# Optimization experiments

Measured on AMD Instinct MI355X. Metric: run time of the kernel, lower is better.

## Reference

```python
import jax, jax.numpy as jnp
import numpy as np

# ---- geometry constants (from init_kwargs) ----
ANGLE_NUM = 360
DET = 448          # detector bins
N = 320            # volume is N x N, voxel pitch 1.0, centered at origin
SID = 500.0        # source-isocenter distance
SDD = 1000.0       # source-detector distance
DU = 1.6           # detector pixel pitch
LAMB = 1.0
R = N * np.sqrt(2.0) / 2.0   # half-diagonal of volume
N_SAMP = 452                 # samples per ray, step ~ 1 voxel
DT = np.float32(2.0 * R / N_SAMP)


def forward_project(vol):
    """Ray-driven fan-beam forward projection. vol: [B,N,N] -> sino [B,A,D]."""
    half = (N - 1) / 2.0
    betas = jnp.deg2rad(jnp.linspace(0.0, 360.0, ANGLE_NUM, endpoint=False)).astype(jnp.float32)
    u = ((jnp.arange(DET, dtype=jnp.float32) - (DET - 1) / 2.0) * DU)          # [D]
    t = (SID - R) + (jnp.arange(N_SAMP, dtype=jnp.float32) + 0.5) * (2.0 * R / N_SAMP)  # [S]

    def one_angle(_, beta):
        cb, sb = jnp.cos(beta), jnp.sin(beta)
        src = jnp.stack([SID * cb, SID * sb])            # source position [2]
        ax = jnp.stack([-cb, -sb])                       # toward isocenter
        uax = jnp.stack([-sb, cb])                       # detector axis
        det_pts = src[None, :] + SDD * ax[None, :] + u[:, None] * uax[None, :]  # [D,2]
        dirs = det_pts - src[None, :]
        dirs = dirs / jnp.linalg.norm(dirs, axis=-1, keepdims=True)             # [D,2]
        pts = src[None, None, :] + t[None, :, None] * dirs[:, None, :]          # [D,S,2]
        ix = pts[..., 0] + half
        iy = pts[..., 1] + half
        x0 = jnp.floor(ix); y0 = jnp.floor(iy)
        fx = ix - x0;       fy = iy - y0
        x0i = x0.astype(jnp.int32); y0i = y0.astype(jnp.int32)

        def gather(yy, xx):
            inb = (xx >= 0) & (xx < N) & (yy >= 0) & (yy < N)
            v = vol[:, jnp.clip(yy, 0, N - 1), jnp.clip(xx, 0, N - 1)]  # [B,D,S]
            return v * inb[None].astype(vol.dtype)

        val = (gather(y0i, x0i)         * ((1 - fx) * (1 - fy))[None]
             + gather(y0i, x0i + 1)     * (fx * (1 - fy))[None]
             + gather(y0i + 1, x0i)     * ((1 - fx) * fy)[None]
             + gather(y0i + 1, x0i + 1) * (fx * fy)[None])
        return None, val.sum(-1) * DT   # line integral per detector bin [B,D]

    _, sino = jax.lax.scan(one_angle, None, betas)   # [A,B,D]
    return jnp.transpose(sino, (1, 0, 2))            # [B,A,D]


def setup_inputs() -> dict:
    key = jax.random.key(0)
    k1, k2 = jax.random.split(key)
    x = jax.random.normal(k1, (2, N, N), dtype=jnp.float32)
    p = jax.random.normal(k2, (2, ANGLE_NUM, DET), dtype=jnp.float32)
    return {"x": x, "p": p}


def reference(x, p):
    # SART-style update: x - lamb * BP(FP(x) - p), BP = exact adjoint of FP
    residual = forward_project(x) - p
    (bp_vol,) = jax.linear_transpose(forward_project, x)(residual)
    return x - LAMB * bp_vol
```

## Files before the change

### kernel.cpp

```cpp
#include <hip/hip_runtime.h>
#include <hip/hip_fp16.h>
#include <math.h>

#define A_NUM 360
#define DET_N 448
#define NN 320
#define NSAMP 452
#define NB 2
#define NPIX (NN * NN)
#define NRAY (A_NUM * DET_N)
#define NCH 4
#define CHS (NSAMP / NCH)
#define NORB 25600
#define NSPQ15 15
#define NSPQ12 12
#define PN 324

#define R_D   226.27416997969522
#define DT_D  (2.0 * R_D / (double)NSAMP)
#define T0_D  (500.0 - R_D + 0.5 * DT_D)
#define DTF   ((float)DT_D)
#define T0F   ((float)T0_D)
#define INVDT ((float)(1.0 / DT_D))
#define K0F   ((float)((-1.4150 - T0_D) * (1.0 / DT_D)))

typedef float f32x2 __attribute__((ext_vector_type(2)));

__device__ __forceinline__ int orb_swizzle(int ri, int rj) {
    int tile = (rj >> 3) * 20 + (ri >> 3);
    int intra = ((rj & 7) << 3) | (ri & 7);
    return (tile << 6) | intra;
}

__global__ __launch_bounds__(256) void prep_k(float2* __restrict__ tabD,
                                              float4* __restrict__ tabS,
                                              float4* __restrict__ dirq,
                                              float4* __restrict__ angG) {
    int tid = blockIdx.x * blockDim.x + threadIdx.x;
    if (tid >= NRAY) return;
    int d = tid % DET_N, a = tid / DET_N;
    double beta = (double)a * (M_PI / 180.0);
    double cbd = cos(beta), sbd = sin(beta);
    double u = ((double)d - 223.5) * 1.6;
    double inorm = 1.0 / sqrt(1.0e6 + u * u);
    float dx = (float)((-1000.0 * cbd - u * sbd) * inorm);
    float dy = (float)((-1000.0 * sbd + u * cbd) * inorm);
    tabD[tid] = make_float2(dx, dy);
    if (d == 0) {
        tabS[a] = make_float4((float)cbd, (float)sbd,
                              (float)(500.0 * cbd + 161.5),
                              (float)(500.0 * sbd + 161.5));
        angG[a] = make_float4((float)cbd, (float)sbd,
                              (float)(500.0 * cbd + 159.5),
                              (float)(500.0 * sbd + 159.5));
    }
    if (a < 90) dirq[a * DET_N + d] = make_float4(dx, dy, DTF * dx, DTF * dy);
}

__device__ __forceinline__ unsigned packpix(const float* __restrict__ x,
                                            bool v, int idx) {
    if (!v) return 0u;
    __half2 h = __floats2half2_rn(x[idx], x[NPIX + idx]);
    return *reinterpret_cast<unsigned*>(&h);
}
__device__ __forceinline__ f32x2 up16(unsigned w) {
    __half2 h = *reinterpret_cast<__half2*>(&w);
    return (f32x2){__low2float(h), __high2float(h)};
}

__global__ __launch_bounds__(256) void interleaveQB_k(const float* __restrict__ x,
                                                      uint4* __restrict__ xb) {
    int t = blockIdx.x * blockDim.x + threadIdx.x;
    if (t >= PN * PN) return;
    int px = t % PN, py = t / PN;
    int ox = px - 2, oy = py - 2;
    bool cx0 = (ox >= 0) && (ox < NN);
    bool cx1 = (ox + 1 >= 0) && (ox + 1 < NN);
    bool cy0 = (oy >= 0) && (oy < NN);
    bool cy1 = (oy + 1 >= 0) && (oy + 1 < NN);
    int b = oy * NN + ox;
    uint4 w;
    w.x = packpix(x, cx0 && cy0, b);
    w.y = packpix(x, cx1 && cy0, b + 1);
    w.z = packpix(x, cx0 && cy1, b + NN);
    w.w = packpix(x, cx1 && cy1, b + NN + 1);
    xb[t] = w;
}

__global__ __launch_bounds__(256) void interleaveQBT_k(const float* __restrict__ x,
                                                       uint4* __restrict__ xbT) {
    int t = blockIdx.x * blockDim.x + threadIdx.x;
    if (t >= PN * PN) return;
    int r = t % PN, q = t / PN;
    int row0 = r - 2, col0 = q - 2;
    bool r0v = (row0 >= 0) && (row0 < NN);
    bool r1v = (row0 + 1 >= 0) && (row0 + 1 < NN);
    bool c0v = (col0 >= 0) && (col0 < NN);
    bool c1v = (col0 + 1 >= 0) && (col0 + 1 < NN);
    int b = row0 * NN + col0;
    uint4 w;
    w.x = packpix(x, r0v && c0v, b);
    w.y = packpix(x, r1v && c0v, b + NN);
    w.z = packpix(x, r0v && c1v, b + 1);
    w.w = packpix(x, r1v && c1v, b + NN + 1);
    xbT[t] = w;
}

__device__ __forceinline__ void samp1(const uint4* __restrict__ buf,
                                      float ix, float iy,
                                      f32x2& accA, f32x2& accB) {
    float xf = floorf(ix), yf = floorf(iy);
    float fx = ix - xf, fy = iy - yf;
    int idx = (int)yf * PN + (int)xf;
    uint4 qv = buf[idx];
    float gx = 1.0f - fx, gy = 1.0f - fy;
    float w00 = gx * gy, w01 = fx * gy, w10 = gx * fy, w11 = fx * fy;
    accA = __builtin_elementwise_fma((f32x2){w00, w00}, up16(qv.x), accA);
    accB = __builtin_elementwise_fma((f32x2){w01, w01}, up16(qv.y), accB);
    accA = __builtin_elementwise_fma((f32x2){w10, w10}, up16(qv.z), accA);
    accB = __builtin_elementwise_fma((f32x2){w11, w11}, up16(qv.w), accB);
}

__global__ __launch_bounds__(256) void partial_k(const float2* __restrict__ tabD,
                                                 const float4* __restrict__ tabS,
                                                 const uint4* __restrict__ bufR,
                                                 const uint4* __restrict__ bufT,
                                                 float2* __restrict__ part) {
    int tid = blockIdx.x * blockDim.x + threadIdx.x;
    if (tid >= NRAY * NCH) return;
    int d_lo = tid & 15;
    int c    = (tid >> 4) & 3;
    int rest = tid >> 6;
    int d_hi = rest % (DET_N / 16);
    int a    = rest / (DET_N / 16);
    int ray  = a * DET_N + d_hi * 16 + d_lo;

    float2 D = tabD[ray];
    float4 S = tabS[a];
    bool swp = fabsf(S.x) > fabsf(S.y);
    float dirx = swp ? D.y : D.x;
    float diry = swp ? D.x : D.y;
    float sx   = swp ? S.w : S.z;
    float sy   = swp ? S.z : S.w;
    const uint4* __restrict__ buf = swp ? bufT : bufR;

    float invx = __builtin_amdgcn_rcpf(dirx);
    float invy = __builtin_amdgcn_rcpf(diry);
    float tx1 = (0.5f   - sx) * invx;
    float tx2 = (322.5f - sx) * invx;
    float ty1 = (0.5f   - sy) * invy;
    float ty2 = (322.5f - sy) * invy;
    float tmn = fmaxf(fminf(tx1, tx2), fminf(ty1, ty2));
    float tmx = fminf(fmaxf(tx1, tx2), fmaxf(ty1, ty2));
    float smnf = fminf(fmaxf(ceilf((tmn - T0F) * INVDT), 0.0f), (float)(NSAMP - 1));
    float smxf = fminf(fmaxf(floorf((tmx - T0F) * INVDT), 0.0f), (float)(NSAMP - 1));
    int smin = (int)smnf;
    int smax = (int)smxf;
    int klo = (smin - c + 3) >> 2;  if (klo < 0) klo = 0;
    int khi = (smax - c) >> 2;      if (khi > CHS - 1) khi = CHS - 1;
    int kn = khi - klo + 1;

    float t0c = fmaf((float)(c + 4 * klo), DTF, T0F);
    float ix = fmaf(t0c, dirx, sx);
    float iy = fmaf(t0c, diry, sy);
    float stx = (4.0f * DTF) * dirx;
    float sty = (4.0f * DTF) * diry;

    f32x2 accA = {0.0f, 0.0f}, accB = {0.0f, 0.0f};

    int k = 0;
#pragma unroll 2
    for (; k + 4 <= kn; k += 4) {
        float ix0 = ix,              iy0 = iy;
        float ix1 = ix + stx,        iy1 = iy + sty;
        float ix2 = ix + 2.0f * stx, iy2 = iy + 2.0f * sty;
        float ix3 = ix + 3.0f * stx, iy3 = iy + 3.0f * sty;
        float xf0 = floorf(ix0), yf0 = floorf(iy0);
        float xf1 = floorf(ix1), yf1 = floorf(iy1);
        float xf2 = floorf(ix2), yf2 = floorf(iy2);
        float xf3 = floorf(ix3), yf3 = floorf(iy3);
        int i0 = (int)yf0 * PN + (int)xf0;
        int i1 = (int)yf1 * PN + (int)xf1;
        int i2 = (int)yf2 * PN + (int)xf2;
        int i3 = (int)yf3 * PN + (int)xf3;
        uint4 q0 = buf[i0];
        uint4 q1 = buf[i1];
        uint4 q2 = buf[i2];
        uint4 q3 = buf[i3];
        float fx0 = ix0 - xf0, fy0 = iy0 - yf0;
        float fx1 = ix1 - xf1, fy1 = iy1 - yf1;
        float fx2 = ix2 - xf2, fy2 = iy2 - yf2;
        float fx3 = ix3 - xf3, fy3 = iy3 - yf3;
        float gx0 = 1.0f - fx0, gy0 = 1.0f - fy0;
        float gx1 = 1.0f - fx1, gy1 = 1.0f - fy1;
        float gx2 = 1.0f - fx2, gy2 = 1.0f - fy2;
        float gx3 = 1.0f - fx3, gy3 = 1.0f - fy3;
        float w;
        w = gx0 * gy0; accA = __builtin_elementwise_fma((f32x2){w, w}, up16(q0.x), accA);
        w = fx0 * gy0; accB = __builtin_elementwise_fma((f32x2){w, w}, up16(q0.y), accB);
        w = gx0 * fy0; accA = __builtin_elementwise_fma((f32x2){w, w}, up16(q0.z), accA);
        w = fx0 * fy0; accB = __builtin_elementwise_fma((f32x2){w, w}, up16(q0.w), accB);
        w = gx1 * gy1; accA = __builtin_elementwise_fma((f32x2){w, w}, up16(q1.x), accA);
        w = fx1 * gy1; accB = __builtin_elementwise_fma((f32x2){w, w}, up16(q1.y), accB);
        w = gx1 * fy1; accA = __builtin_elementwise_fma((f32x2){w, w}, up16(q1.z), accA);
        w = fx1 * fy1; accB = __builtin_elementwise_fma((f32x2){w, w}, up16(q1.w), accB);
        w = gx2 * gy2; accA = __builtin_elementwise_fma((f32x2){w, w}, up16(q2.x), accA);
        w = fx2 * gy2; accB = __builtin_elementwise_fma((f32x2){w, w}, up16(q2.y), accB);
        w = gx2 * fy2; accA = __builtin_elementwise_fma((f32x2){w, w}, up16(q2.z), accA);
        w = fx2 * fy2; accB = __builtin_elementwise_fma((f32x2){w, w}, up16(q2.w), accB);
        w = gx3 * gy3; accA = __builtin_elementwise_fma((f32x2){w, w}, up16(q3.x), accA);
        w = fx3 * gy3; accB = __builtin_elementwise_fma((f32x2){w, w}, up16(q3.y), accB);
        w = gx3 * fy3; accA = __builtin_elementwise_fma((f32x2){w, w}, up16(q3.z), accA);
        w = fx3 * fy3; accB = __builtin_elementwise_fma((f32x2){w, w}, up16(q3.w), accB);
        ix += 4.0f * stx; iy += 4.0f * sty;
    }
    for (; k < kn; ++k) {
        samp1(buf, ix, iy, accA, accB);
        ix += stx; iy += sty;
    }

    f32x2 acc = accA + accB;
    part[c * NRAY + ray] = make_float2(acc.x, acc.y);
}

__global__ __launch_bounds__(256) void finalize4_k(const float* __restrict__ p,
                                                   const float2* __restrict__ part,
                                                   float4* __restrict__ rvq) {
    int tid = blockIdx.x * blockDim.x + threadIdx.x;
    if (tid >= 90 * DET_N) return;
    int d = tid % DET_N, am = tid / DET_N;
    float rv[8];
#pragma unroll
    for (int k = 0; k < 4; ++k) {
        int ray = (am + 90 * k) * DET_N + d;
        float a0 = 0.0f, a1 = 0.0f;
#pragma unroll
        for (int c = 0; c < NCH; ++c) {
            float2 pr = part[c * NRAY + ray];
            a0 += pr.x; a1 += pr.y;
        }
        rv[2 * k]     = -fmaf(a0, DTF, -p[ray]) * DTF;
        rv[2 * k + 1] = -fmaf(a1, DTF, -p[NRAY + ray]) * DTF;
    }
    rvq[2 * tid]     = make_float4(rv[0], rv[1], rv[2], rv[3]);
    rvq[2 * tid + 1] = make_float4(rv[4], rv[5], rv[6], rv[7]);
}

#define TAP4(A0, A1, A2, A3)                                 \
    {                                                        \
        f32x2 ad  = __builtin_elementwise_max(dxy, -dxy);    \
        f32x2 wv2 = __builtin_elementwise_max(one2 - ad, zero2); \
        float w = wv2.x * wv2.y;                             \
        f32x2 wv = {w, w};                                   \
        A0 = __builtin_elementwise_fma(wv, q0, A0);          \
        A1 = __builtin_elementwise_fma(wv, q1, A1);          \
        A2 = __builtin_elementwise_fma(wv, q2, A2);          \
        A3 = __builtin_elementwise_fma(wv, q3, A3);          \
        dxy += dd2;                                          \
    }

#define QBODY(A0, A1, A2, A3, Q, DX_, DY_, EX_, EY_)                       \
    for (int am = sp; am < 90; am += NSPLIT) {                             \
        int a = 90 * (Q) + am;                                             \
        float4 A = ang[a];                                                 \
        float rx = fi - A.z, ry = fj - A.w;                                \
        float rpar  = -fmaf(rx, A.x, ry * A.y);                            \
        float rperp = fmaf(ry, A.x, -rx * A.y);                            \
        float us = 1000.0f * rperp * __builtin_amdgcn_rcpf(rpar);          \
        float dstar = fmaf(us, 0.625f, 223.5f);                            \
        float r2 = fmaf(rx, rx, ry * ry);                                  \
        float ir = rsqrtf(r2);                                             \
        float g  = fmaf(fabsf(rx) + fabsf(ry), ir, 0.031f);                \
        float kk = fmaf(us, us, 1.0e6f) * ir;                              \
        float dd = fmaf(g * kk, 6.25e-4f, 0.05f);                          \
        int dlo = (int)ceilf(dstar - dd);  if (dlo < 0) dlo = 0;           \
        int dhi = (int)floorf(dstar + dd); if (dhi > DET_N - 1) dhi = DET_N - 1; \
        const float4* Drow = dirq + am * DET_N;                            \
        const float4* Rrow = rvq + am * DET_N * 2;                         \
        for (int d = dlo; d <= dhi; ++d) {                                 \
            float4 Dq  = Drow[d];                                          \
            float4 r01 = Rrow[2 * d];                                      \
            float4 r23 = Rrow[2 * d + 1];                                  \
            float Tx = DX_, Ty = DY_;                                      \
            float ts = fmaf(rx, Tx, ry * Ty);                              \
            float sf = ceilf(fmaf(ts, INVDT, K0F));                        \
            sf = fminf(fmaxf(sf, 0.0f), (float)(NSAMP - 3));               \
            float tt = fmaf(sf, DTF, T0F);                                 \
            f32x2 dxy = {fmaf(tt, Tx, -rx), fmaf(tt, Ty, -ry)};            \
            f32x2 dd2 = {EX_, EY_};                                        \
            f32x2 q0 = {r01.x, r01.y}, q1 = {r01.z, r01.w};                \
            f32x2 q2 = {r23.x, r23.y}, q3 = {r23.z, r23.w};                \
            TAP4(A0, A1, A2, A3)                                           \
            TAP4(A0, A1, A2, A3)                                           \
            TAP4(A0, A1, A2, A3)                                           \
        }                                                                  \
    }

template <int NSPLIT>
__global__ __launch_bounds__(256) void bp4_k(const float4* __restrict__ dirq,
                                             const float4* __restrict__ rvq,
                                             const float4* __restrict__ angG,
                                             float* __restrict__ bpp) {
    __shared__ float4 ang[A_NUM];
    for (int a = threadIdx.x; a < A_NUM; a += blockDim.x) ang[a] = angG[a];
    __syncthreads();

    int tid = blockIdx.x * blockDim.x + threadIdx.x;
    if (tid >= NORB * NSPLIT) return;
    int orb = tid % NORB;
    int sp  = tid / NORB;
    int tile  = orb >> 6;
    int intra = orb & 63;
    int ri = (tile % 20) * 8 + (intra & 7);
    int rj = (tile / 20) * 8 + (intra >> 3);
    float fi = (float)ri, fj = (float)rj;

    const f32x2 one2 = {1.0f, 1.0f}, zero2 = {0.0f, 0.0f};
    f32x2 acc0 = {0.0f, 0.0f}, acc1 = acc0, acc2 = acc0, acc3 = acc0;

    QBODY(acc0, acc1, acc2, acc3, 0,  Dq.x,  Dq.y,  Dq.z,  Dq.w)
    QBODY(acc3, acc0, acc1, acc2, 1, -Dq.y,  Dq.x, -Dq.w,  Dq.z)
    QBODY(acc2, acc3, acc0, acc1, 2, -Dq.x, -Dq.y, -Dq.z, -Dq.w)
    QBODY(acc1, acc2, acc3, acc0, 3,  Dq.y, -Dq.x,  Dq.w, -Dq.z)

    int base = sp * 8 * NORB + orb;
    bpp[base           ] = acc0.x;
    bpp[base + 1 * NORB] = acc0.y;
    bpp[base + 2 * NORB] = acc1.x;
    bpp[base + 3 * NORB] = acc1.y;
    bpp[base + 4 * NORB] = acc2.x;
    bpp[base + 5 * NORB] = acc2.y;
    bpp[base + 6 * NORB] = acc3.x;
    bpp[base + 7 * NORB] = acc3.y;
}

template <int NSPLIT>
__global__ __launch_bounds__(256) void combine4_k(const float* __restrict__ x,
                                                  const float* __restrict__ bpp,
                                                  float* __restrict__ out) {
    int tid = blockIdx.x * blockDim.x + threadIdx.x;
    if (tid >= NB * NPIX) return;
    int i = tid % NN;
    int j = (tid / NN) % NN;
    int b = tid / NPIX;
    int k, ri, rj;
    if (j < 160) {
        if (i < 160) { k = 0; ri = i;       rj = j;       }
        else         { k = 1; ri = j;       rj = 319 - i; }
    } else {
        if (i >= 160){ k = 2; ri = 319 - i; rj = 319 - j; }
        else         { k = 3; ri = 319 - j; rj = i;       }
    }
    int off = (k * 2 + b) * NORB + orb_swizzle(ri, rj);
    float s = x[tid];
#pragma unroll
    for (int sp = 0; sp < NSPLIT; ++sp) s += bpp[sp * 8 * NORB + off];
    out[tid] = s;
}

template <bool USE_TAB>
__global__ __launch_bounds__(256) void residual_k(const float* __restrict__ x,
                                                  const float* __restrict__ p,
                                                  void* __restrict__ tabv) {
    int tid = blockIdx.x * blockDim.x + threadIdx.x;
    if (tid >= NRAY) return;
    int d = tid % DET_N, a = tid / DET_N;
    double beta = (double)a * (M_PI / 180.0);
    double cbd = cos(beta), sbd = sin(beta);
    double u = ((double)d - 223.5) * 1.6;
    double inorm = 1.0 / sqrt(1.0e6 + u * u);
    float dirx = (float)((-1000.0 * cbd - u * sbd) * inorm);
    float diry = (float)((-1000.0 * sbd + u * cbd) * inorm);
    float sx = (float)(500.0 * cbd + 159.5);
    float sy = (float)(500.0 * sbd + 159.5);
    const float* __restrict__ v0 = x;
    const float* __restrict__ v1 = x + NPIX;
    float acc0 = 0.0f, acc1 = 0.0f;
    for (int s = 0; s < NSAMP; ++s) {
        float t  = fmaf((float)s, DTF, T0F);
        float ix = fmaf(t, dirx, sx);
        float iy = fmaf(t, diry, sy);
        float xf = floorf(ix), yf = floorf(iy);
        int x0 = (int)xf, y0 = (int)yf;
        if (x0 < -1 || x0 >= NN || y0 < -1 || y0 >= NN) continue;
        float fx = ix - xf, fy = iy - yf;
        int x1 = x0 + 1, y1 = y0 + 1;
        bool vx0 = (x0 >= 0), vx1 = (x1 < NN);
        bool vy0 = (y0 >= 0), vy1 = (y1 < NN);
        int x0c = vx0 ? x0 : 0, x1c = vx1 ? x1 : NN - 1;
        int y0c = vy0 ? y0 : 0, y1c = vy1 ? y1 : NN - 1;
        int i00 = y0c * NN + x0c, i01 = y0c * NN + x1c;
        int i10 = y1c * NN + x0c, i11 = y1c * NN + x1c;
        float gx = 1.0f - fx, gy = 1.0f - fy;
        float w00 = (vx0 && vy0) ? gx * gy : 0.0f;
        float w01 = (vx1 && vy0) ? fx * gy : 0.0f;
        float w10 = (vx0 && vy1) ? gx * fy : 0.0f;
        float w11 = (vx1 && vy1) ? fx * fy : 0.0f;
        acc0 = fmaf(v0[i00], w00, acc0); acc0 = fmaf(v0[i01], w01, acc0);
        acc0 = fmaf(v0[i10], w10, acc0); acc0 = fmaf(v0[i11], w11, acc0);
        acc1 = fmaf(v1[i00], w00, acc1); acc1 = fmaf(v1[i01], w01, acc1);
        acc1 = fmaf(v1[i10], w10, acc1); acc1 = fmaf(v1[i11], w11, acc1);
    }
    float rv0 = -fmaf(acc0, DTF, -p[tid]) * DTF;
    float rv1 = -fmaf(acc1, DTF, -p[NRAY + tid]) * DTF;
    if constexpr (USE_TAB) {
        ((float4*)tabv)[tid] = make_float4(dirx, diry, rv0, rv1);
    } else {
        ((float2*)tabv)[tid] = make_float2(rv0, rv1);
    }
}

template <int NSPLIT, bool DIRECT, bool USE_TAB>
__global__ __launch_bounds__(256) void bp_k(const void* __restrict__ tabv,
                                            const float* __restrict__ x,
                                            float* __restrict__ outp) {
    __shared__ float4 ang[A_NUM];
    for (int a = threadIdx.x; a < A_NUM; a += blockDim.x) {
        double beta = (double)a * (M_PI / 180.0);
        double cbd = cos(beta), sbd = sin(beta);
        ang[a] = make_float4((float)cbd, (float)sbd,
                             (float)(500.0 * cbd + 159.5),
                             (float)(500.0 * sbd + 159.5));
    }
    __syncthreads();

    int tid = blockIdx.x * blockDim.x + threadIdx.x;
    if (tid >= NPIX * NSPLIT) return;
    int pix = tid % NPIX;
    int sp  = tid / NPIX;
    float fi = (float)(pix % NN), fj = (float)(pix / NN);

    float acc0 = 0.0f, acc1 = 0.0f;

    for (int a = sp; a < A_NUM; a += NSPLIT) {
        float4 A = ang[a];
        float rx = fi - A.z, ry = fj - A.w;
        float rpar  = -fmaf(rx, A.x, ry * A.y);
        float rperp = fmaf(ry, A.x, -rx * A.y);
        float us = 1000.0f * rperp * __builtin_amdgcn_rcpf(rpar);
        float dstar = fmaf(us, 0.625f, 223.5f);
        float r2 = fmaf(rx, rx, ry * ry);
        float kk = fmaf(us, us, 1.0e6f) * rsqrtf(r2);
        float dd = fmaf(kk, 8.8394e-4f, 0.05f);
        int dlo = (int)ceilf(dstar - dd);  if (dlo < 0) dlo = 0;
        int dhi = (int)floorf(dstar + dd); if (dhi > DET_N - 1) dhi = DET_N - 1;

        const float4* __restrict__ Trow =
            USE_TAB ? ((const float4*)tabv) + a * DET_N : nullptr;
        const float2* __restrict__ RVrow =
            USE_TAB ? nullptr : ((const float2*)tabv) + a * DET_N;

        for (int d = dlo; d <= dhi; ++d) {
            float dirx, diry, rv0, rv1;
            if constexpr (USE_TAB) {
                float4 T = Trow[d];
                dirx = T.x; diry = T.y; rv0 = T.z; rv1 = T.w;
            } else {
                float u = ((float)d - 223.5f) * 1.6f;
                float inv = rsqrtf(fmaf(u, u, 1.0e6f));
                dirx = fmaf(-1000.0f, A.x, -u * A.y) * inv;
                diry = fmaf(-1000.0f, A.y,  u * A.x) * inv;
                float2 RV = RVrow[d];
                rv0 = RV.x; rv1 = RV.y;
            }
            float ts = fmaf(rx, dirx, ry * diry);
            float sf = ceilf(fmaf(ts, INVDT, K0F));
            sf = fminf(fmaxf(sf, 0.0f), (float)(NSAMP - 3));
            float tt = fmaf(sf, DTF, T0F);
            float dx = fmaf(tt, dirx, -rx);
            float dy = fmaf(tt, diry, -ry);
            float ddx = DTF * dirx, ddy = DTF * diry;
#pragma unroll
            for (int k = 0; k < 3; ++k) {
                float wx = fmaxf(1.0f - fabsf(dx), 0.0f);
                float wy = fmaxf(1.0f - fabsf(dy), 0.0f);
                float w = wx * wy;
                acc0 = fmaf(w, rv0, acc0);
                acc1 = fmaf(w, rv1, acc1);
                dx += ddx; dy += ddy;
            }
        }
    }

    if constexpr (DIRECT) {
        outp[pix]        = x[pix]        + acc0;
        outp[NPIX + pix] = x[NPIX + pix] + acc1;
    } else {
        outp[(sp * 2 + 0) * NPIX + pix] = acc0;
        outp[(sp * 2 + 1) * NPIX + pix] = acc1;
    }
}

template <int NSPLIT>
__global__ __launch_bounds__(256) void combine_k(const float* __restrict__ x,
                                                 const float* __restrict__ part,
                                                 float* __restrict__ out) {
    int tid = blockIdx.x * blockDim.x + threadIdx.x;
    if (tid >= NB * NPIX) return;
    int pix = tid % NPIX, b = tid / NPIX;
    float s = x[tid];
#pragma unroll
    for (int sp = 0; sp < NSPLIT; ++sp) s += part[(sp * 2 + b) * NPIX + pix];
    out[tid] = s;
}

extern "C" void kernel_launch(void* const* d_in, const int* in_sizes, int n_in,
                              void* d_out, int out_size, void* d_ws, size_t ws_size,
                              hipStream_t stream) {
    const float* x = (const float*)d_in[0];
    const float* p = (const float*)d_in[1];
    float* out = (float*)d_out;
    char* ws = (char*)d_ws;

    const size_t bpp15_bytes = (size_t)NSPQ15 * 8 * NORB * 4;
    const size_t bpp12_bytes = (size_t)NSPQ12 * 8 * NORB * 4;
    const size_t NEED15 = 1951744 + bpp15_bytes;
    const size_t NEED12 = 1951744 + bpp12_bytes;
    const size_t NEED8  = 10471936;

    const size_t tab_bytes  = sizeof(float4) * NRAY;
    const size_t bpp4_bytes = sizeof(float) * 8 * NPIX;

    if (ws_size >= NEED12 || ws_size >= NEED8) {
        float4* dirq  = (float4*)(ws + 0);
        float2* tabD  = (float2*)(ws + 645120);
        float4* rvq   = (float4*)(ws + 645120);
        float4* tabS  = (float4*)(ws + 1935360);
        float4* angG  = (float4*)(ws + 1943552);
        uint4*  xqb   = (uint4*)(ws + 1951744);
        uint4*  xqbT  = (uint4*)(ws + 3631360);
        float2* fpart = (float2*)(ws + 5310976);
        float*  bpp   = (float*)(ws + 1951744);

        prep_k<<<NRAY / 256, 256, 0, stream>>>(tabD, tabS, dirq, angG);
        interleaveQB_k<<<(PN * PN + 255) / 256, 256, 0, stream>>>(x, xqb);
        interleaveQBT_k<<<(PN * PN + 255) / 256, 256, 0, stream>>>(x, xqbT);
        partial_k<<<(NRAY * NCH) / 256, 256, 0, stream>>>(tabD, tabS, xqb, xqbT, fpart);
        finalize4_k<<<(90 * DET_N + 255) / 256, 256, 0, stream>>>(p, fpart, rvq);
        if (ws_size >= NEED15) {
            bp4_k<NSPQ15><<<(NORB * NSPQ15) / 256, 256, 0, stream>>>(dirq, rvq, angG, bpp);
            combine4_k<NSPQ15><<<(NB * NPIX) / 256, 256, 0, stream>>>(x, bpp, out);
        } else if (ws_size >= NEED12) {
            bp4_k<NSPQ12><<<(NORB * NSPQ12) / 256, 256, 0, stream>>>(dirq, rvq, angG, bpp);
            combine4_k<NSPQ12><<<(NB * NPIX) / 256, 256, 0, stream>>>(x, bpp, out);
        } else {
            bp4_k<8><<<(NORB * 8) / 256, 256, 0, stream>>>(dirq, rvq, angG, bpp);
            combine4_k<8><<<(NB * NPIX) / 256, 256, 0, stream>>>(x, bpp, out);
        }
    } else if (ws_size >= tab_bytes + bpp4_bytes) {
        float4* tab = (float4*)ws;
        float* bpp  = (float*)(ws + tab_bytes);
        residual_k<true><<<(NRAY + 255) / 256, 256, 0, stream>>>(x, p, tab);
        bp_k<4, false, true><<<(NPIX * 4) / 256, 256, 0, stream>>>(tab, x, bpp);
        combine_k<4><<<(NB * NPIX + 255) / 256, 256, 0, stream>>>(x, bpp, out);
    } else if (ws_size >= tab_bytes) {
        float4* tab = (float4*)ws;
        residual_k<true><<<(NRAY + 255) / 256, 256, 0, stream>>>(x, p, tab);
        bp_k<1, true, true><<<NPIX / 256, 256, 0, stream>>>(tab, x, out);
    } else {
        float2* rw2 = (float2*)ws;
        residual_k<false><<<(NRAY + 255) / 256, 256, 0, stream>>>(x, p, rw2);
        bp_k<1, true, false><<<NPIX / 256, 256, 0, stream>>>(rw2, x, out);
    }
}
```

Before: 147.8 us.

## Stage per-angle detector tables in LDS and interleave quadrants per angle

The backprojection kernel now loops over angle index once and, for each angle, cooperatively loads the direction and ray-value tables for all 448 detectors into shared memory. It then processes all four symmetric quadrants from those LDS copies instead of issuing scattered global loads per detector. This trades global/L2 gather traffic for two block barriers per angle. It also removes the early return, which relies on the grid exactly covering NORB*NSPLIT threads so that every thread reaches the barriers.

New measurement: 142.0 us. 1.04x faster.

```diff
diff --git a/kernel.cpp b/kernel.cpp
--- a/kernel.cpp
+++ b/kernel.cpp
@@ -259,10 +259,9 @@
         dxy += dd2;                                          \
     }
 
-#define QBODY(A0, A1, A2, A3, Q, DX_, DY_, EX_, EY_)                       \
-    for (int am = sp; am < 90; am += NSPLIT) {                             \
-        int a = 90 * (Q) + am;                                             \
-        float4 A = ang[a];                                                 \
+#define QTAPS(Q, A0, A1, A2, A3, DX_, DY_, EX_, EY_)                       \
+    {                                                                      \
+        float4 A = sAng[90 * (Q) + am];                                    \
         float rx = fi - A.z, ry = fj - A.w;                                \
         float rpar  = -fmaf(rx, A.x, ry * A.y);                            \
         float rperp = fmaf(ry, A.x, -rx * A.y);                            \
@@ -275,12 +274,10 @@
         float dd = fmaf(g * kk, 6.25e-4f, 0.05f);                          \
         int dlo = (int)ceilf(dstar - dd);  if (dlo < 0) dlo = 0;           \
         int dhi = (int)floorf(dstar + dd); if (dhi > DET_N - 1) dhi = DET_N - 1; \
-        const float4* Drow = dirq + am * DET_N;                            \
-        const float4* Rrow = rvq + am * DET_N * 2;                         \
         for (int d = dlo; d <= dhi; ++d) {                                 \
-            float4 Dq  = Drow[d];                                          \
-            float4 r01 = Rrow[2 * d];                                      \
-            float4 r23 = Rrow[2 * d + 1];                                  \
+            float4 Dq  = sD[d];                                            \
+            float4 r01 = sR0[d];                                           \
+            float4 r23 = sR1[d];                                           \
             float Tx = DX_, Ty = DY_;                                      \
             float ts = fmaf(rx, Tx, ry * Ty);                              \
             float sf = ceilf(fmaf(ts, INVDT, K0F));                        \
@@ -301,12 +298,13 @@
                                              const float4* __restrict__ rvq,
                                              const float4* __restrict__ angG,
                                              float* __restrict__ bpp) {
-    __shared__ float4 ang[A_NUM];
-    for (int a = threadIdx.x; a < A_NUM; a += blockDim.x) ang[a] = angG[a];
-    __syncthreads();
-
-    int tid = blockIdx.x * blockDim.x + threadIdx.x;
-    if (tid >= NORB * NSPLIT) return;
+    __shared__ float4 sAng[A_NUM];
+    __shared__ float4 sD[DET_N];
+    __shared__ float4 sR0[DET_N];
+    __shared__ float4 sR1[DET_N];
+    for (int a = threadIdx.x; a < A_NUM; a += blockDim.x) sAng[a] = angG[a];
+
+    int tid = blockIdx.x * blockDim.x + threadIdx.x;
     int orb = tid % NORB;
     int sp  = tid / NORB;
     int tile  = orb >> 6;
@@ -318,10 +316,22 @@
     const f32x2 one2 = {1.0f, 1.0f}, zero2 = {0.0f, 0.0f};
     f32x2 acc0 = {0.0f, 0.0f}, acc1 = acc0, acc2 = acc0, acc3 = acc0;
 
-    QBODY(acc0, acc1, acc2, acc3, 0,  Dq.x,  Dq.y,  Dq.z,  Dq.w)
-    QBODY(acc3, acc0, acc1, acc2, 1, -Dq.y,  Dq.x, -Dq.w,  Dq.z)
-    QBODY(acc2, acc3, acc0, acc1, 2, -Dq.x, -Dq.y, -Dq.z, -Dq.w)
-    QBODY(acc1, acc2, acc3, acc0, 3,  Dq.y, -Dq.x,  Dq.w, -Dq.z)
+    for (int am = sp; am < 90; am += NSPLIT) {
+        const float4* Drow = dirq + am * DET_N;
+        const float4* Rrow = rvq + am * DET_N * 2;
+        __syncthreads();
+        for (int i = threadIdx.x; i < DET_N; i += 256) {
+            sD[i]  = Drow[i];
+            sR0[i] = Rrow[2 * i];
+            sR1[i] = Rrow[2 * i + 1];
+        }
+        __syncthreads();
+
+        QTAPS(0, acc0, acc1, acc2, acc3,  Dq.x,  Dq.y,  Dq.z,  Dq.w)
+        QTAPS(1, acc3, acc0, acc1, acc2, -Dq.y,  Dq.x, -Dq.w,  Dq.z)
+        QTAPS(2, acc2, acc3, acc0, acc1, -Dq.x, -Dq.y, -Dq.z, -Dq.w)
+        QTAPS(3, acc1, acc2, acc3, acc0,  Dq.y, -Dq.x,  Dq.w, -Dq.z)
+    }
 
     int base = sp * 8 * NORB + orb;
     bpp[base           ] = acc0.x;
```
